# Optimization experiments

Hardware: AMD Instinct MI355X
Metric: run time of the kernel (lower is better)

## Reference

```python
import jax, jax.numpy as jnp
import numpy as np

DROP_P = 0.1  # module default dropout


def setup_inputs() -> dict:
    key = jax.random.key(0)
    kq, kk, kv = jax.random.split(key, 3)
    B, L, H = 4, 4096, 64
    return {
        "q": jax.random.normal(kq, (B, L, H), dtype=jnp.float32),
        "k": jax.random.normal(kk, (B, L, H), dtype=jnp.float32),
        "v": jax.random.normal(kv, (B, L, H), dtype=jnp.float32),
    }


def reference(q, k, v):
    # q: [B, ql, H], k: [B, kl, H], v: [B, kl, H]
    H = q.shape[-1]
    scale = 1.0 / jnp.sqrt(jnp.asarray(H, dtype=q.dtype))
    # [B, ql, kl] score matrix (materialized, as in the original module)
    scores = jnp.einsum('bqh,bkh->bqk', q, k) * scale
    ql, kl = scores.shape[1], scores.shape[2]
    causal = jnp.tril(jnp.ones((ql, kl), dtype=bool))  # self.tril[:ql, :kl]
    scores = jnp.where(causal[None, :, :], scores, -jnp.inf)
    wei = jax.nn.softmax(scores, axis=-1)
    # deterministic dropout (train-mode path in the torch module)
    keep_p = 1.0 - DROP_P
    keep = jax.random.bernoulli(jax.random.key(42), keep_p, wei.shape)
    wei = jnp.where(keep, wei / keep_p, jnp.zeros((), dtype=wei.dtype))
    return jnp.einsum('bqk,bkh->bqh', wei, v)
```

## Files before the change

### kernel.cpp

```cpp
#include <hip/hip_runtime.h>

#define LQ   4096
#define HDIM 64
#define KEEP_LIMIT (7549747u << 9)

typedef __attribute__((ext_vector_type(8))) short short8v;
typedef __attribute__((ext_vector_type(4))) short short4v;
typedef __attribute__((ext_vector_type(4))) float f32x4;

__device__ __forceinline__ unsigned rotl32(unsigned x, int r) {
  return (x << r) | (x >> (32 - r));
}

__device__ __forceinline__ float keep_sel(unsigned j, float e) {
  const unsigned ks1 = 42u;
  const unsigned ks2 = 0x1BD11BDAu ^ 42u;
  unsigned x0 = 0u, x1 = j + ks1;
#define TFR(r) { x0 += x1; x1 = rotl32(x1, r); x1 ^= x0; }
  TFR(13) TFR(15) TFR(26) TFR(6)   x0 += ks1; x1 += ks2 + 1u;
  TFR(17) TFR(29) TFR(16) TFR(24)  x0 += ks2; x1 += 0u  + 2u;
  TFR(13) TFR(15) TFR(26) TFR(6)   x0 += 0u;  x1 += ks1 + 3u;
  TFR(17) TFR(29) TFR(16) TFR(24)  x0 += ks1; x1 += ks2 + 4u;
  TFR(13) TFR(15) TFR(26) TFR(6)   x0 += ks2; x1 += 0u  + 5u;
#undef TFR
  return ((x0 ^ x1) < KEEP_LIMIT) ? e : 0.f;
}

__device__ __forceinline__ unsigned short f2bf(float x) {
  unsigned u = __float_as_uint(x);
  u += 0x7fffu + ((u >> 16) & 1u);
  return (unsigned short)(u >> 16);
}

__device__ __forceinline__ void gload16(const void* g, void* l) {
  __builtin_amdgcn_global_load_lds(
      (const __attribute__((address_space(1))) unsigned int*)g,
      (__attribute__((address_space(3))) unsigned int*)l, 16, 0, 0);
}

#if __has_builtin(__builtin_amdgcn_mfma_f32_16x16x16bf16_1k)
#define MFMA16(a, b, c) __builtin_amdgcn_mfma_f32_16x16x16bf16_1k(a, b, c, 0, 0, 0)
#else
__device__ __forceinline__ f32x4 mfma16_asm(short4v a, short4v b, f32x4 c) {
  f32x4 d;
  asm volatile("v_mfma_f32_16x16x16_bf16 %0, %1, %2, %3"
               : "=v"(d) : "v"(a), "v"(b), "v"(c));
  return d;
}
#define MFMA16(a, b, c) mfma16_asm(a, b, c)
#endif

__global__ __launch_bounds__(256) void prep(const float* __restrict__ k,
                                            const float* __restrict__ v,
                                            unsigned short* __restrict__ kb,
                                            unsigned short* __restrict__ vtb) {
  __shared__ float t[64][65];
  const int b = blockIdx.y, tl = blockIdx.x;
  const int tid = threadIdx.x, lane = tid & 63, grp = tid >> 6;
  {
    const float* kp = k + ((size_t)b * LQ + tl * 64) * HDIM;
    unsigned short* kbp = kb + ((size_t)b * LQ + tl * 64) * HDIM;
#pragma unroll
    for (int i = 0; i < 4; i++) {
      int e = (i * 256 + tid) * 4;
      float4 x = *(const float4*)(kp + e);
      ushort4 y;
      y.x = f2bf(x.x); y.y = f2bf(x.y); y.z = f2bf(x.z); y.w = f2bf(x.w);
      *(ushort4*)(kbp + e) = y;
    }
  }
#pragma unroll
  for (int c = 0; c < 16; c++) {
    int r = c * 4 + grp;
    t[r][lane] = v[((size_t)b * LQ + tl * 64 + r) * HDIM + lane];
  }
  __syncthreads();
#pragma unroll
  for (int c = 0; c < 16; c++) {
    int h = c * 4 + grp;
    vtb[((size_t)b * HDIM + h) * LQ + tl * 64 + lane] = f2bf(t[lane][h]);
  }
}

__global__ __launch_bounds__(256, 4) void attn(
    const float* __restrict__ q, const unsigned short* __restrict__ kb,
    const unsigned short* __restrict__ vtb, float* __restrict__ o) {
  __shared__ __align__(16) unsigned short kl[2][64 * 64];
  __shared__ __align__(16) unsigned short vl[2][64 * 64];
  __shared__ float lsq[4][16];

  const int bx = blockIdx.x;
  const int tile16 = 255 - (bx >> 2);
  const int b = bx & 3;
  const int tid = threadIdx.x, lane = tid & 63, wq = tid >> 6;
  const int g = lane >> 4, r = lane & 15;
  const int qrow = tile16 * 16 + r;
  const int nt = (tile16 >> 2) + 1;
  const unsigned sw = (unsigned)((r & 7) << 4);

  short8v qf0, qf1;
  {
    const float* qp = q + ((size_t)b * LQ + qrow) * HDIM + g * 8;
    float4 a0 = *(const float4*)qp;
    float4 a1 = *(const float4*)(qp + 4);
    float4 b0 = *(const float4*)(qp + 32);
    float4 b1 = *(const float4*)(qp + 36);
    qf0[0] = (short)f2bf(a0.x); qf0[1] = (short)f2bf(a0.y);
    qf0[2] = (short)f2bf(a0.z); qf0[3] = (short)f2bf(a0.w);
    qf0[4] = (short)f2bf(a1.x); qf0[5] = (short)f2bf(a1.y);
    qf0[6] = (short)f2bf(a1.z); qf0[7] = (short)f2bf(a1.w);
    qf1[0] = (short)f2bf(b0.x); qf1[1] = (short)f2bf(b0.y);
    qf1[2] = (short)f2bf(b0.z); qf1[3] = (short)f2bf(b0.w);
    qf1[4] = (short)f2bf(b1.x); qf1[5] = (short)f2bf(b1.y);
    qf1[6] = (short)f2bf(b1.z); qf1[7] = (short)f2bf(b1.w);
  }

#define STAGE(T, BI)                                                           \
  {                                                                            \
    size_t kgb = ((size_t)b * LQ + (size_t)(T) * 64) * 128;                    \
    _Pragma("unroll") for (int it = 0; it < 2; ++it) {                         \
      unsigned d = (unsigned)(it * 4096 + tid * 16);                           \
      unsigned so = (d & ~127u) | ((d & 127u) ^ (((d >> 7) & 7u) << 4));       \
      gload16((const char*)kb + kgb + so,                                      \
              (char*)&kl[BI][0] + (wq * 1024 + it * 4096));                    \
    }                                                                          \
    _Pragma("unroll") for (int it = 0; it < 2; ++it) {                         \
      unsigned d = (unsigned)(it * 4096 + tid * 16);                           \
      unsigned row = d >> 7, col = d & 127u;                                   \
      size_t vgb = ((size_t)b * HDIM + row) * (LQ * 2) +                       \
                   (size_t)(T) * 128 + (col ^ ((row & 7u) << 4));              \
      gload16((const char*)vtb + vgb,                                          \
              (char*)&vl[BI][0] + (wq * 1024 + it * 4096));                    \
    }                                                                          \
  }

  f32x4 acc[4];
  acc[0] = (f32x4){0, 0, 0, 0}; acc[1] = (f32x4){0, 0, 0, 0};
  acc[2] = (f32x4){0, 0, 0, 0}; acc[3] = (f32x4){0, 0, 0, 0};
  float lsum = 0.f;

  STAGE(0, 0)
  __syncthreads();

  for (int t = 0; t < nt; ++t) {
    const int bi = t & 1;
    if (t + 1 < nt) STAGE(t + 1, bi ^ 1)

    const char* klp = (const char*)&kl[bi][0] + (wq * 16 + r) * 128;
    short8v kf0 = *(const short8v*)(klp + ((unsigned)(g * 16) ^ sw));
    short8v kf1 = *(const short8v*)(klp + ((unsigned)(g * 16 + 64) ^ sw));

    f32x4 S = __builtin_amdgcn_mfma_f32_16x16x32_bf16(kf0, qf0,
                                                      (f32x4){0, 0, 0, 0}, 0, 0, 0);
    S = __builtin_amdgcn_mfma_f32_16x16x32_bf16(kf1, qf1, S, 0, 0, 0);

    short4v pa;
    const int kvb = t * 64 + wq * 16 + g * 4;
    const unsigned jbase =
        ((unsigned)b << 24) | ((unsigned)qrow << 12) | (unsigned)kvb;
#pragma unroll
    for (int reg = 0; reg < 4; ++reg) {
      float e = (kvb + reg <= qrow) ? __expf(S[reg] * 0.125f) : 0.f;
      lsum += e;
      float w = keep_sel(jbase + (unsigned)reg, e);
      pa[reg] = (short)f2bf(w);
    }

    const char* vlp = (const char*)&vl[bi][0];
#pragma unroll
    for (int hg = 0; hg < 4; ++hg) {
      short4v vf = *(const short4v*)(vlp + (hg * 16 + r) * 128 +
                                     ((unsigned)(wq * 32 + g * 8) ^ sw));
      acc[hg] = MFMA16(pa, vf, acc[hg]);
    }
    __syncthreads();
  }
#undef STAGE

  float s = lsum;
  s += __shfl_xor(s, 16);
  s += __shfl_xor(s, 32);
  if (lane < 16) lsq[wq][lane] = s;

  float* obuf = (float*)&kl[0][0];
#pragma unroll
  for (int hg = 0; hg < 4; ++hg)
#pragma unroll
    for (int reg = 0; reg < 4; ++reg)
      obuf[(wq * 16 + g * 4 + reg) * 64 + hg * 16 + r] = acc[hg][reg];
  __syncthreads();

  const int i = tid >> 4, h4 = tid & 15;
  f32x4 vs = (f32x4){0, 0, 0, 0};
#pragma unroll
  for (int qq = 0; qq < 4; ++qq)
    vs += *(const f32x4*)&obuf[(qq * 16 + i) * 64 + h4 * 4];
  float ls = lsq[0][i] + lsq[1][i] + lsq[2][i] + lsq[3][i];
  float inv = 1.0f / (ls * 0.9f);
  float4 outv;
  outv.x = vs[0] * inv; outv.y = vs[1] * inv;
  outv.z = vs[2] * inv; outv.w = vs[3] * inv;
  *(float4*)&o[((size_t)b * LQ + tile16 * 16 + i) * HDIM + h4 * 4] = outv;
}

extern "C" void kernel_launch(void* const* d_in, const int* in_sizes, int n_in,
                              void* d_out, int out_size, void* d_ws, size_t ws_size,
                              hipStream_t stream) {
  const float* q = (const float*)d_in[0];
  const float* k = (const float*)d_in[1];
  const float* v = (const float*)d_in[2];
  float* out = (float*)d_out;
  unsigned short* kb  = (unsigned short*)d_ws;
  unsigned short* vtb = kb + (size_t)4 * LQ * HDIM;

  prep<<<dim3(64, 4), 256, 0, stream>>>(k, v, kb, vtb);
  attn<<<1024, 256, 0, stream>>>(q, kb, vtb, out);
}
```

Before: 101.6 us.

## Split KV range across two blocks with atomic reduction and separate normalize pass

Each query tile's causal KV range is now split between two blocks, doubling the grid. Partial outputs and row sums are combined with global atomics into zeroed buffers, and a new kernel applies the normalization. K is read straight from global into registers with prefetch instead of being staged in LDS, which lets occupancy rise to 8 blocks per CU. The causal mask now runs only on the diagonal tile, and exp2 plus a packed bf16 convert shorten the softmax path. The cost is two memsets, an extra launch, heavy atomic traffic on the output, and nondeterministic summation order.

```diff
diff --git a/kernel.cpp b/kernel.cpp
--- a/kernel.cpp
+++ b/kernel.cpp
@@ -3,6 +3,7 @@
 #define LQ   4096
 #define HDIM 64
 #define KEEP_LIMIT (7549747u << 9)
+#define SCALE_LOG2E 0.18033688011112042f
 
 typedef __attribute__((ext_vector_type(8))) short short8v;
 typedef __attribute__((ext_vector_type(4))) short short4v;
@@ -82,20 +83,23 @@
   }
 }
 
-__global__ __launch_bounds__(256, 4) void attn(
+__global__ __launch_bounds__(256, 8) void attn(
     const float* __restrict__ q, const unsigned short* __restrict__ kb,
-    const unsigned short* __restrict__ vtb, float* __restrict__ o) {
-  __shared__ __align__(16) unsigned short kl[2][64 * 64];
+    const unsigned short* __restrict__ vtb, float* __restrict__ o,
+    float* __restrict__ plsum) {
   __shared__ __align__(16) unsigned short vl[2][64 * 64];
-  __shared__ float lsq[4][16];
 
   const int bx = blockIdx.x;
-  const int tile16 = 255 - (bx >> 2);
-  const int b = bx & 3;
+  const int tile16 = 255 - (bx >> 3);
+  const int b = (bx >> 1) & 3;
+  const int s = bx & 1;
   const int tid = threadIdx.x, lane = tid & 63, wq = tid >> 6;
   const int g = lane >> 4, r = lane & 15;
   const int qrow = tile16 * 16 + r;
   const int nt = (tile16 >> 2) + 1;
+  const int half = (nt + 1) >> 1;
+  const int ts = s ? half : 0, te = s ? nt : half;
+  const int ntm1 = nt - 1;
   const unsigned sw = (unsigned)((r & 7) << 4);
 
   short8v qf0, qf1;
@@ -115,23 +119,23 @@
     qf1[6] = (short)f2bf(b1.z); qf1[7] = (short)f2bf(b1.w);
   }
 
+  const char* vt_b = (const char*)vtb + (size_t)b * HDIM * LQ * 2;
+  unsigned vsrc0, vsrc1;
+  {
+    unsigned d0 = (unsigned)(tid * 16);
+    unsigned d1 = d0 + 4096u;
+    vsrc0 = (d0 >> 7) * (LQ * 2) + ((d0 & 127u) ^ (((d0 >> 7) & 7u) << 4));
+    vsrc1 = (d1 >> 7) * (LQ * 2) + ((d1 & 127u) ^ (((d1 >> 7) & 7u) << 4));
+  }
+  const char* kbl =
+      (const char*)kb + ((size_t)b * LQ + wq * 16 + r) * 128 + g * 16;
+
 #define STAGE(T, BI)                                                           \
   {                                                                            \
-    size_t kgb = ((size_t)b * LQ + (size_t)(T) * 64) * 128;                    \
-    _Pragma("unroll") for (int it = 0; it < 2; ++it) {                         \
-      unsigned d = (unsigned)(it * 4096 + tid * 16);                           \
-      unsigned so = (d & ~127u) | ((d & 127u) ^ (((d >> 7) & 7u) << 4));       \
-      gload16((const char*)kb + kgb + so,                                      \
-              (char*)&kl[BI][0] + (wq * 1024 + it * 4096));                    \
-    }                                                                          \
-    _Pragma("unroll") for (int it = 0; it < 2; ++it) {                         \
-      unsigned d = (unsigned)(it * 4096 + tid * 16);                           \
-      unsigned row = d >> 7, col = d & 127u;                                   \
-      size_t vgb = ((size_t)b * HDIM + row) * (LQ * 2) +                       \
-                   (size_t)(T) * 128 + (col ^ ((row & 7u) << 4));              \
-      gload16((const char*)vtb + vgb,                                          \
-              (char*)&vl[BI][0] + (wq * 1024 + it * 4096));                    \
-    }                                                                          \
+    gload16(vt_b + vsrc0 + (size_t)(T) * 128,                                  \
+            (char*)&vl[BI][0] + wq * 1024);                                    \
+    gload16(vt_b + vsrc1 + (size_t)(T) * 128,                                  \
+            (char*)&vl[BI][0] + wq * 1024 + 4096);                             \
   }
 
   f32x4 acc[4];
@@ -139,68 +143,84 @@
   acc[2] = (f32x4){0, 0, 0, 0}; acc[3] = (f32x4){0, 0, 0, 0};
   float lsum = 0.f;
 
-  STAGE(0, 0)
+  short8v k0c, k1c;
+  if (ts < te) {
+    STAGE(ts, 0)
+    k0c = *(const short8v*)(kbl + (size_t)ts * 8192);
+    k1c = *(const short8v*)(kbl + (size_t)ts * 8192 + 64);
+  }
   __syncthreads();
 
-  for (int t = 0; t < nt; ++t) {
-    const int bi = t & 1;
-    if (t + 1 < nt) STAGE(t + 1, bi ^ 1)
-
-    const char* klp = (const char*)&kl[bi][0] + (wq * 16 + r) * 128;
-    short8v kf0 = *(const short8v*)(klp + ((unsigned)(g * 16) ^ sw));
-    short8v kf1 = *(const short8v*)(klp + ((unsigned)(g * 16 + 64) ^ sw));
-
-    f32x4 S = __builtin_amdgcn_mfma_f32_16x16x32_bf16(kf0, qf0,
+  for (int t = ts; t < te; ++t) {
+    const int bi = (t - ts) & 1;
+    short8v k0n, k1n;
+    const bool more = (t + 1 < te);
+    if (more) {
+      STAGE(t + 1, bi ^ 1)
+      k0n = *(const short8v*)(kbl + (size_t)(t + 1) * 8192);
+      k1n = *(const short8v*)(kbl + (size_t)(t + 1) * 8192 + 64);
+    }
+
+    f32x4 S = __builtin_amdgcn_mfma_f32_16x16x32_bf16(k0c, qf0,
                                                       (f32x4){0, 0, 0, 0}, 0, 0, 0);
-    S = __builtin_amdgcn_mfma_f32_16x16x32_bf16(kf1, qf1, S, 0, 0, 0);
-
-    short4v pa;
+    S = __builtin_amdgcn_mfma_f32_16x16x32_bf16(k1c, qf1, S, 0, 0, 0);
+
     const int kvb = t * 64 + wq * 16 + g * 4;
-    const unsigned jbase =
+    const unsigned jb =
         ((unsigned)b << 24) | ((unsigned)qrow << 12) | (unsigned)kvb;
-#pragma unroll
-    for (int reg = 0; reg < 4; ++reg) {
-      float e = (kvb + reg <= qrow) ? __expf(S[reg] * 0.125f) : 0.f;
-      lsum += e;
-      float w = keep_sel(jbase + (unsigned)reg, e);
-      pa[reg] = (short)f2bf(w);
-    }
-
-    const char* vlp = (const char*)&vl[bi][0];
+    float w[4];
+    if (t == ntm1) {
+#pragma unroll
+      for (int reg = 0; reg < 4; ++reg) {
+        float e = (kvb + reg <= qrow) ? exp2f(S[reg] * SCALE_LOG2E) : 0.f;
+        lsum += e;
+        w[reg] = keep_sel(jb + (unsigned)reg, e);
+      }
+    } else {
+#pragma unroll
+      for (int reg = 0; reg < 4; ++reg) {
+        float e = exp2f(S[reg] * SCALE_LOG2E);
+        lsum += e;
+        w[reg] = keep_sel(jb + (unsigned)reg, e);
+      }
+    }
+
+    union { unsigned u[2]; short4v s4; } pu;
+    asm("v_cvt_pk_bf16_f32 %0, %1, %2" : "=v"(pu.u[0]) : "v"(w[0]), "v"(w[1]));
+    asm("v_cvt_pk_bf16_f32 %0, %1, %2" : "=v"(pu.u[1]) : "v"(w[2]), "v"(w[3]));
+    const short4v pa = pu.s4;
+
+    const char* vlp = (const char*)&vl[bi][0] + r * 128 +
+                      (((unsigned)(wq * 32 + g * 8)) ^ sw);
 #pragma unroll
     for (int hg = 0; hg < 4; ++hg) {
-      short4v vf = *(const short4v*)(vlp + (hg * 16 + r) * 128 +
-                                     ((unsigned)(wq * 32 + g * 8) ^ sw));
+      short4v vf = *(const short4v*)(vlp + hg * 2048);
       acc[hg] = MFMA16(pa, vf, acc[hg]);
     }
     __syncthreads();
+    if (more) { k0c = k0n; k1c = k1n; }
   }
 #undef STAGE
 
-  float s = lsum;
-  s += __shfl_xor(s, 16);
-  s += __shfl_xor(s, 32);
-  if (lane < 16) lsq[wq][lane] = s;
-
-  float* obuf = (float*)&kl[0][0];
+  lsum += __shfl_xor(lsum, 16);
+  lsum += __shfl_xor(lsum, 32);
+  if (lane < 16)
+    atomicAdd(&plsum[b * LQ + tile16 * 16 + lane], lsum);
+
+  float* ob = o + ((size_t)b * LQ + tile16 * 16) * HDIM;
 #pragma unroll
   for (int hg = 0; hg < 4; ++hg)
 #pragma unroll
     for (int reg = 0; reg < 4; ++reg)
-      obuf[(wq * 16 + g * 4 + reg) * 64 + hg * 16 + r] = acc[hg][reg];
-  __syncthreads();
-
-  const int i = tid >> 4, h4 = tid & 15;
-  f32x4 vs = (f32x4){0, 0, 0, 0};
-#pragma unroll
-  for (int qq = 0; qq < 4; ++qq)
-    vs += *(const f32x4*)&obuf[(qq * 16 + i) * 64 + h4 * 4];
-  float ls = lsq[0][i] + lsq[1][i] + lsq[2][i] + lsq[3][i];
-  float inv = 1.0f / (ls * 0.9f);
-  float4 outv;
-  outv.x = vs[0] * inv; outv.y = vs[1] * inv;
-  outv.z = vs[2] * inv; outv.w = vs[3] * inv;
-  *(float4*)&o[((size_t)b * LQ + tile16 * 16 + i) * HDIM + h4 * 4] = outv;
+      atomicAdd(&ob[(g * 4 + reg) * HDIM + hg * 16 + r], acc[hg][reg]);
+}
+
+__global__ __launch_bounds__(256) void norm(float* __restrict__ o,
+                                            const float* __restrict__ plsum) {
+  const int idx = blockIdx.x * 256 + threadIdx.x;
+  f32x4 x = ((const f32x4*)o)[idx];
+  const float inv = 1.0f / (plsum[idx >> 4] * 0.9f);
+  ((f32x4*)o)[idx] = x * inv;
 }
 
 extern "C" void kernel_launch(void* const* d_in, const int* in_sizes, int n_in,
@@ -212,7 +232,11 @@
   float* out = (float*)d_out;
   unsigned short* kb  = (unsigned short*)d_ws;
   unsigned short* vtb = kb + (size_t)4 * LQ * HDIM;
-
+  float* plsum = (float*)((char*)d_ws + (size_t)4 * 1024 * 1024);
+
+  hipMemsetAsync(out, 0, (size_t)4 * LQ * HDIM * sizeof(float), stream);
+  hipMemsetAsync(plsum, 0, (size_t)4 * LQ * sizeof(float), stream);
   prep<<<dim3(64, 4), 256, 0, stream>>>(k, v, kb, vtb);
-  attn<<<1024, 256, 0, stream>>>(q, kb, vtb, out);
-}
+  attn<<<2048, 256, 0, stream>>>(q, kb, vtb, out, plsum);
+  norm<<<1024, 256, 0, stream>>>(out, plsum);
+}
```

Result: slower. 108.4 us (+6.7%).
